# Performance work log

Measured on AMD Instinct MI355X. Metric: run time of the kernel, lower is better.

The kernel has to match this reference:

```python
import jax, jax.numpy as jnp
import numpy as np

BATCH = 8
MAX_SEQ = 2048
HEAD_NUM = 16  # num_attention_heads_per_partition


def setup_inputs() -> dict:
    key = jax.random.key(0)
    k1, k2 = jax.random.split(key)
    attention_mask = jax.random.uniform(k1, (BATCH, 1, MAX_SEQ, MAX_SEQ), dtype=jnp.float16)
    # ragged per-sequence lengths in [1, MAX_SEQ]; concrete (shape params, not traced)
    seq_lengths = np.asarray(jax.random.randint(k2, (BATCH,), 1, MAX_SEQ + 1), dtype=np.int32)
    return {"attention_mask": attention_mask, "seq_lengths": seq_lengths}


def reference(attention_mask, seq_lengths):
    # Pack the top-left s_i x s_i block of each batch's mask, replicated across
    # HEAD_NUM heads, into one flat fp16 buffer; then threshold > 0.5 -> bool.
    mask = attention_mask.astype(jnp.float16)
    lens = [int(s) for s in np.asarray(seq_lengths)]  # static shape params
    pieces = []
    for i, s in enumerate(lens):
        block = mask[i, 0, :s, :s]                        # [s, s]
        rep = jnp.broadcast_to(block, (HEAD_NUM, s, s))   # replicate per head
        pieces.append(rep.reshape(-1))                    # [HEAD_NUM*s*s]
    packed = jnp.concatenate(pieces)                      # [sum_i HEAD_NUM*s_i^2]
    return packed > jnp.float16(0.5)
```

## Files before the change

### kernel.cpp

```cpp
#include <hip/hip_runtime.h>

typedef int i4 __attribute__((ext_vector_type(4)));
typedef int i2 __attribute__((ext_vector_type(2)));

#define NTS4(P, V) __builtin_nontemporal_store((V), (i4*)(P))
#define NTS2(P, V) __builtin_nontemporal_store((V), (i2*)(P))
#define NTS1(P, V) __builtin_nontemporal_store((V), (P))

#define THREADS 256
#define WAVES_PB 4
#define ITERS 2
#define MAX_BLOCKS 4096

__global__ void setup_offsets_kernel(const int* __restrict__ seq,
                                     unsigned int* __restrict__ ws) {
    if (threadIdx.x == 0 && blockIdx.x == 0) {
        unsigned int o16 = 0, cs = 0;
        ws[0] = 0u; ws[9] = 0u;
        for (int b = 0; b < 8; ++b) {
            unsigned int s  = (unsigned int)seq[b];
            unsigned int s2 = s * s;
            o16 += 16u * s2;
            cs  += (s2 + 1023u) >> 10;
            ws[1 + b]  = o16;
            ws[10 + b] = cs;
            ws[18 + b] = s;
            ws[26 + b] = s2;
            ((float*)ws)[34 + b] = 1.0f / (float)s;
        }
    }
}

#define STORE_SHIFT(VV, SIG) do {                                              \
    NTS4(out + offh + 0   + (SIG), VV[0]);                                     \
    NTS4(out + offh + 256 + (SIG), VV[1]);                                     \
    NTS4(out + offh + 512 + (SIG), VV[2]);                                     \
    if (lane < 63u) NTS4(out + offh + 768 + (SIG), VV[3]);                     \
    if (lane == 0u) {                                                          \
        NTS1(out + habase, o[0].x);                                            \
        if ((SIG) >= 2) NTS1(out + habase + 1, o[0].y);                        \
        if ((SIG) == 3) NTS1(out + habase + 2, o[0].z);                        \
    }                                                                          \
    if (lane == 63u) {                                                         \
        if ((SIG) == 1) NTS1(out + habase + 1021, o[3].y);                     \
        if ((SIG) <= 2) NTS1(out + habase + 1022, o[3].z);                     \
        NTS1(out + habase + 1023, o[3].w);                                     \
    }                                                                          \
} while (0)

__global__ void __launch_bounds__(THREADS)
unpad_mask_kernel(const float* __restrict__ mask,
                  const unsigned int* __restrict__ ws,
                  int* __restrict__ out) {
    __shared__ unsigned int off16[9];
    __shared__ unsigned int csum[9];
    __shared__ unsigned int slen[8];
    __shared__ unsigned int ssq[8];
    __shared__ float        sinv[8];

    int tx = threadIdx.x;
    if (tx < 9) { off16[tx] = ws[tx]; csum[tx] = ws[9 + tx]; }
    if (tx < 8) {
        slen[tx] = ws[18 + tx];
        ssq[tx]  = ws[26 + tx];
        sinv[tx] = ((const float*)ws)[34 + tx];
    }
    __syncthreads();

    unsigned int nchunks     = csum[8];
    unsigned int total_waves = gridDim.x * WAVES_PB;
    unsigned int wave_id     = blockIdx.x * WAVES_PB + ((unsigned int)tx >> 6);
    unsigned int lane        = (unsigned int)tx & 63u;

#pragma unroll 1
    for (int it = 0; it < ITERS; ++it) {
        unsigned int chunk = wave_id + (unsigned int)it * total_waves;
        if (chunk >= nchunks) break;

        unsigned int b = 0;
#pragma unroll
        for (int j = 1; j < 8; ++j) b += (chunk >= csum[j]) ? 1u : 0u;

        unsigned int s    = slen[b];
        unsigned int s2   = ssq[b];
        float        inv  = sinv[b];
        unsigned int p0   = (chunk - csum[b]) << 10;
        unsigned int base = off16[b];
        const float* mb   = mask + ((size_t)b << 22);

        if (s2 - p0 >= 1024u) {
            unsigned int q0 = p0 + (lane << 2);
            i4 o[4];
#pragma unroll
            for (int sub = 0; sub < 4; ++sub) {
                unsigned int q   = q0 + ((unsigned int)sub << 8);
                unsigned int row = (unsigned int)((float)q * inv);
                int col = (int)q - (int)(row * s);
                if (col < 0)            { row -= 1u; col += (int)s; }
                else if (col >= (int)s) { row += 1u; col -= (int)s; }

                unsigned int r0 = row;  int c0 = col;
                float v0 = mb[(size_t)r0 * 2048u + (unsigned int)c0];
                c0++; if (c0 == (int)s) { c0 = 0; r0++; }
                float v1 = mb[(size_t)r0 * 2048u + (unsigned int)c0];
                c0++; if (c0 == (int)s) { c0 = 0; r0++; }
                float v2 = mb[(size_t)r0 * 2048u + (unsigned int)c0];
                c0++; if (c0 == (int)s) { c0 = 0; r0++; }
                float v3 = mb[(size_t)r0 * 2048u + (unsigned int)c0];

                o[sub] = (i4){(v0 > 0.5f) ? 1 : 0,
                              (v1 > 0.5f) ? 1 : 0,
                              (v2 > 0.5f) ? 1 : 0,
                              (v3 > 0.5f) ? 1 : 0};
            }

            if ((s & 1u) == 0u) {
                unsigned int off = base + q0;
#pragma unroll
                for (int h = 0; h < 16; ++h) {
                    NTS4(out + off,       o[0]);
                    NTS4(out + off + 256, o[1]);
                    NTS4(out + off + 512, o[2]);
                    NTS4(out + off + 768, o[3]);
                    off += s2;
                }
            } else {
                int src = ((int)lane + 1) & 63;
                int sel = (lane == 0u) ? 1 : 0;
                int e0x = sel ? o[1].x : o[0].x;
                int e0y = sel ? o[1].y : o[0].y;
                int e0z = sel ? o[1].z : o[0].z;
                int e1x = sel ? o[2].x : o[1].x;
                int e1y = sel ? o[2].y : o[1].y;
                int e1z = sel ? o[2].z : o[1].z;
                int e2x = sel ? o[3].x : o[2].x;
                int e2y = sel ? o[3].y : o[2].y;
                int e2z = sel ? o[3].z : o[2].z;
                int n0x = __shfl(e0x, src, 64), n0y = __shfl(e0y, src, 64), n0z = __shfl(e0z, src, 64);
                int n1x = __shfl(e1x, src, 64), n1y = __shfl(e1y, src, 64), n1z = __shfl(e1z, src, 64);
                int n2x = __shfl(e2x, src, 64), n2y = __shfl(e2y, src, 64), n2z = __shfl(e2z, src, 64);
                int n3x = __shfl(o[3].x, src, 64), n3y = __shfl(o[3].y, src, 64), n3z = __shfl(o[3].z, src, 64);

                i4 v1[4], v2[4], v3[4];
                v1[0] = (i4){o[0].y, o[0].z, o[0].w, n0x};
                v1[1] = (i4){o[1].y, o[1].z, o[1].w, n1x};
                v1[2] = (i4){o[2].y, o[2].z, o[2].w, n2x};
                v1[3] = (i4){o[3].y, o[3].z, o[3].w, n3x};
                v2[0] = (i4){o[0].z, o[0].w, n0x, n0y};
                v2[1] = (i4){o[1].z, o[1].w, n1x, n1y};
                v2[2] = (i4){o[2].z, o[2].w, n2x, n2y};
                v2[3] = (i4){o[3].z, o[3].w, n3x, n3y};
                v3[0] = (i4){o[0].w, n0x, n0y, n0z};
                v3[1] = (i4){o[1].w, n1x, n1y, n1z};
                v3[2] = (i4){o[2].w, n2x, n2y, n2z};
                v3[3] = (i4){o[3].w, n3x, n3y, n3z};

                unsigned int habase = base + p0;
#pragma unroll
                for (int h = 0; h < 16; ++h) {
                    unsigned int offh = habase + (lane << 2);
                    const int r0c = h & 3;
                    if (r0c == 0) {
                        NTS4(out + offh,       o[0]);
                        NTS4(out + offh + 256, o[1]);
                        NTS4(out + offh + 512, o[2]);
                        NTS4(out + offh + 768, o[3]);
                    } else if (r0c == 1) {
                        STORE_SHIFT(v3, 3);
                    } else if (r0c == 2) {
                        STORE_SHIFT(v2, 2);
                    } else {
                        STORE_SHIFT(v1, 1);
                    }
                    habase += s2;
                }
            }
        } else {
#pragma unroll 1
            for (int sub = 0; sub < 4; ++sub) {
                unsigned int sp0 = p0 + ((unsigned int)sub << 8);
                if (sp0 >= s2) break;

                if (s2 - sp0 >= 256u) {
                    unsigned int q   = sp0 + (lane << 2);
                    unsigned int row = (unsigned int)((float)q * inv);
                    int col = (int)q - (int)(row * s);
                    if (col < 0)            { row -= 1u; col += (int)s; }
                    else if (col >= (int)s) { row += 1u; col -= (int)s; }

                    unsigned int r0 = row;  int c0 = col;
                    float v0 = mb[(size_t)r0 * 2048u + (unsigned int)c0];
                    c0++; if (c0 == (int)s) { c0 = 0; r0++; }
                    float v1 = mb[(size_t)r0 * 2048u + (unsigned int)c0];
                    c0++; if (c0 == (int)s) { c0 = 0; r0++; }
                    float v2 = mb[(size_t)r0 * 2048u + (unsigned int)c0];
                    c0++; if (c0 == (int)s) { c0 = 0; r0++; }
                    float v3 = mb[(size_t)r0 * 2048u + (unsigned int)c0];

                    int o0 = (v0 > 0.5f) ? 1 : 0;
                    int o1 = (v1 > 0.5f) ? 1 : 0;
                    int o2 = (v2 > 0.5f) ? 1 : 0;
                    int o3 = (v3 > 0.5f) ? 1 : 0;
                    i4 o4  = (i4){o0, o1, o2, o3};
                    i2 o2a = (i2){o0, o1};
                    i2 o2b = (i2){o2, o3};

                    unsigned int off = base + q;
                    if ((s & 1u) == 0u) {
#pragma unroll
                        for (int h = 0; h < 16; ++h) {
                            NTS4(out + off, o4);
                            off += s2;
                        }
                    } else {
#pragma unroll
                        for (int h = 0; h < 16; ++h) {
                            if ((h & 3) == 0) {
                                NTS4(out + off, o4);
                            } else if ((h & 3) == 2) {
                                NTS2(out + off,     o2a);
                                NTS2(out + off + 2, o2b);
                            } else {
                                NTS1(out + off,     o0);
                                NTS1(out + off + 1, o1);
                                NTS1(out + off + 2, o2);
                                NTS1(out + off + 3, o3);
                            }
                            off += s2;
                        }
                    }
                } else {
#pragma unroll
                    for (int j = 0; j < 4; ++j) {
                        unsigned int p = sp0 + (lane << 2) + (unsigned int)j;
                        if (p >= s2) continue;
                        unsigned int row = (unsigned int)((float)p * inv);
                        int col = (int)p - (int)(row * s);
                        if (col < 0)            { row -= 1u; col += (int)s; }
                        else if (col >= (int)s) { row += 1u; col -= (int)s; }
                        float v = mb[(size_t)row * 2048u + (unsigned int)col];
                        int o = (v > 0.5f) ? 1 : 0;
                        unsigned int off = base + p;
#pragma unroll
                        for (int h = 0; h < 16; ++h) {
                            NTS1(out + off, o);
                            off += s2;
                        }
                    }
                }
            }
        }
    }
}

extern "C" void kernel_launch(void* const* d_in, const int* in_sizes, int n_in,
                              void* d_out, int out_size, void* d_ws, size_t ws_size,
                              hipStream_t stream) {
    const float*  mask = (const float*)d_in[0];
    const int*    seq  = (const int*)d_in[1];
    unsigned int* ws   = (unsigned int*)d_ws;
    int*          out  = (int*)d_out;

    setup_offsets_kernel<<<1, 64, 0, stream>>>(seq, ws);
    unpad_mask_kernel<<<MAX_BLOCKS, THREADS, 0, stream>>>(mask, ws, out);
}
```

Measured before the change: 680.6 us.

## Split mask unpad into pack pass and aligned per-head fanout copy kernel

Replaces the single fused kernel with two passes when workspace is large enough. The first pass thresholds and packs each sequence's mask block into a compact workspace buffer, and the second copies it out to all 16 head positions using aligned 16-byte output stores with scalar edge handling. This avoids the misaligned shuffle and split-store paths for odd sequence lengths, at the cost of an extra kernel launch and a packed intermediate that is written and then re-read. It also swaps the nontemporal stores for ordinary stores, and the old fused kernel stays as a fallback.

```diff
diff --git a/kernel.cpp b/kernel.cpp
--- a/kernel.cpp
+++ b/kernel.cpp
@@ -1,16 +1,16 @@
 #include <hip/hip_runtime.h>
 
-typedef int i4 __attribute__((ext_vector_type(4)));
-typedef int i2 __attribute__((ext_vector_type(2)));
-
-#define NTS4(P, V) __builtin_nontemporal_store((V), (i4*)(P))
-#define NTS2(P, V) __builtin_nontemporal_store((V), (i2*)(P))
-#define NTS1(P, V) __builtin_nontemporal_store((V), (P))
+typedef int i4  __attribute__((ext_vector_type(4)));
+typedef int i2  __attribute__((ext_vector_type(2)));
+typedef int i4u __attribute__((ext_vector_type(4), aligned(4)));
 
 #define THREADS 256
 #define WAVES_PB 4
-#define ITERS 2
-#define MAX_BLOCKS 4096
+#define K1_BLOCKS 4096
+#define K1_ITERS 2
+#define K2_BLOCKS 8192
+#define PK_OFF 256
+#define WS_NEED ((size_t)4 * (PK_OFF + 32768u * 1024u))
 
 __global__ void setup_offsets_kernel(const int* __restrict__ seq,
                                      unsigned int* __restrict__ ws) {
@@ -31,27 +31,157 @@
     }
 }
 
+
+__global__ void __launch_bounds__(THREADS)
+pack_kernel(const float* __restrict__ mask, const unsigned int* __restrict__ ws,
+            int* __restrict__ pk) {
+    __shared__ unsigned int csum[9];
+    __shared__ unsigned int slen[8];
+    __shared__ unsigned int ssq[8];
+    __shared__ float        sinv[8];
+    int tx = threadIdx.x;
+    if (tx < 9) csum[tx] = ws[9 + tx];
+    if (tx < 8) {
+        slen[tx] = ws[18 + tx];
+        ssq[tx]  = ws[26 + tx];
+        sinv[tx] = ((const float*)ws)[34 + tx];
+    }
+    __syncthreads();
+
+    unsigned int nchunks     = csum[8];
+    unsigned int total_waves = gridDim.x * WAVES_PB;
+    unsigned int wave_id     = blockIdx.x * WAVES_PB + ((unsigned int)tx >> 6);
+    unsigned int lane        = (unsigned int)tx & 63u;
+
+#pragma unroll 1
+    for (int it = 0; it < K1_ITERS; ++it) {
+        unsigned int chunk = wave_id + (unsigned int)it * total_waves;
+        if (chunk >= nchunks) break;
+
+        unsigned int b = 0;
+#pragma unroll
+        for (int j = 1; j < 8; ++j) b += (chunk >= csum[j]) ? 1u : 0u;
+
+        unsigned int s   = slen[b];
+        unsigned int s2  = ssq[b];
+        float        inv = sinv[b];
+        unsigned int p0  = (chunk - csum[b]) << 10;
+        unsigned int pb  = csum[b] << 10;
+        const float* mb  = mask + ((size_t)b << 22);
+
+#pragma unroll
+        for (int sub = 0; sub < 4; ++sub) {
+            unsigned int p = p0 + ((unsigned int)sub << 8) + (lane << 2);
+            if (p + 4u <= s2) {
+                unsigned int row = (unsigned int)((float)p * inv);
+                int col = (int)p - (int)(row * s);
+                if (col < 0)            { row -= 1u; col += (int)s; }
+                else if (col >= (int)s) { row += 1u; col -= (int)s; }
+                unsigned int r0 = row;  int c0 = col;
+                float v0 = mb[(size_t)r0 * 2048u + (unsigned int)c0];
+                c0++; if (c0 == (int)s) { c0 = 0; r0++; }
+                float v1 = mb[(size_t)r0 * 2048u + (unsigned int)c0];
+                c0++; if (c0 == (int)s) { c0 = 0; r0++; }
+                float v2 = mb[(size_t)r0 * 2048u + (unsigned int)c0];
+                c0++; if (c0 == (int)s) { c0 = 0; r0++; }
+                float v3 = mb[(size_t)r0 * 2048u + (unsigned int)c0];
+                i4 o = (i4){(v0 > 0.5f) ? 1 : 0, (v1 > 0.5f) ? 1 : 0,
+                            (v2 > 0.5f) ? 1 : 0, (v3 > 0.5f) ? 1 : 0};
+                *(i4*)(pk + pb + p) = o;
+            } else {
+#pragma unroll
+                for (int j = 0; j < 4; ++j) {
+                    unsigned int pp = p + (unsigned int)j;
+                    if (pp >= s2) continue;
+                    unsigned int row = (unsigned int)((float)pp * inv);
+                    int col = (int)pp - (int)(row * s);
+                    if (col < 0)            { row -= 1u; col += (int)s; }
+                    else if (col >= (int)s) { row += 1u; col -= (int)s; }
+                    float v = mb[(size_t)row * 2048u + (unsigned int)col];
+                    pk[pb + pp] = (v > 0.5f) ? 1 : 0;
+                }
+            }
+        }
+    }
+}
+
+__global__ void __launch_bounds__(THREADS)
+fanout_kernel(const unsigned int* __restrict__ ws, const int* __restrict__ pk,
+              int* __restrict__ out) {
+    __shared__ unsigned int off16[9];
+    __shared__ unsigned int csum[9];
+    __shared__ unsigned int ssq[8];
+    int tx = threadIdx.x;
+    if (tx < 9) { off16[tx] = ws[tx]; csum[tx] = ws[9 + tx]; }
+    if (tx < 8) ssq[tx] = ws[26 + tx];
+    __syncthreads();
+
+    unsigned int nitems      = csum[8] << 4;
+    unsigned int total_waves = gridDim.x * WAVES_PB;
+    unsigned int W           = blockIdx.x * WAVES_PB + ((unsigned int)tx >> 6);
+    unsigned int lane        = (unsigned int)tx & 63u;
+
+#pragma unroll 1
+    for (unsigned int item = W; item < nitems; item += total_waves) {
+        unsigned int cid = item >> 4;
+        unsigned int h   = item & 15u;
+
+        unsigned int b = 0;
+#pragma unroll
+        for (int j = 1; j < 8; ++j) b += (cid >= csum[j]) ? 1u : 0u;
+
+        unsigned int s2 = ssq[b];
+        unsigned int c  = cid - csum[b];
+        const int*  srcb = pk + (csum[b] << 10);
+
+        unsigned int hb   = off16[b] + h * s2;
+        unsigned int lo   = hb + (c << 10);
+        unsigned int clen = s2 - (c << 10);
+        if (clen > 1024u) clen = 1024u;
+        unsigned int hi = lo + clen;
+
+        unsigned int qs = (lo + 3u) >> 2;
+        unsigned int qe = hi >> 2;
+
+#pragma unroll
+        for (int k = 0; k < 4; ++k) {
+            unsigned int q = qs + lane + ((unsigned int)k << 6);
+            if (q < qe) {
+                i4 v = *(const i4u*)(srcb + ((q << 2) - hb));
+                *(i4*)(out + ((size_t)q << 2)) = v;
+            }
+        }
+        if (lane < 3u) {
+            unsigned int e = lo + lane;
+            if (e < hi && e < (qs << 2)) out[e] = srcb[e - hb];
+            unsigned int e2 = (qe << 2) + lane;
+            if (e2 >= lo && e2 < hi) out[e2] = srcb[e2 - hb];
+        }
+    }
+}
+
+
 #define STORE_SHIFT(VV, SIG) do {                                              \
-    NTS4(out + offh + 0   + (SIG), VV[0]);                                     \
-    NTS4(out + offh + 256 + (SIG), VV[1]);                                     \
-    NTS4(out + offh + 512 + (SIG), VV[2]);                                     \
-    if (lane < 63u) NTS4(out + offh + 768 + (SIG), VV[3]);                     \
+    *(i4*)(out + offh + 0   + (SIG)) = VV[0];                                  \
+    *(i4*)(out + offh + 256 + (SIG)) = VV[1];                                  \
+    *(i4*)(out + offh + 512 + (SIG)) = VV[2];                                  \
+    if (lane < 63u) *(i4*)(out + offh + 768 + (SIG)) = VV[3];                  \
     if (lane == 0u) {                                                          \
-        NTS1(out + habase, o[0].x);                                            \
-        if ((SIG) >= 2) NTS1(out + habase + 1, o[0].y);                        \
-        if ((SIG) == 3) NTS1(out + habase + 2, o[0].z);                        \
+        out[habase] = o[0].x;                                                  \
+        if ((SIG) >= 2) out[habase + 1] = o[0].y;                              \
+        if ((SIG) == 3) out[habase + 2] = o[0].z;                              \
     }                                                                          \
     if (lane == 63u) {                                                         \
-        if ((SIG) == 1) NTS1(out + habase + 1021, o[3].y);                     \
-        if ((SIG) <= 2) NTS1(out + habase + 1022, o[3].z);                     \
-        NTS1(out + habase + 1023, o[3].w);                                     \
+        if ((SIG) == 1) out[habase + 1021] = o[3].y;                           \
+        if ((SIG) <= 2) out[habase + 1022] = o[3].z;                           \
+        out[habase + 1023] = o[3].w;                                           \
     }                                                                          \
 } while (0)
 
 __global__ void __launch_bounds__(THREADS)
-unpad_mask_kernel(const float* __restrict__ mask,
-                  const unsigned int* __restrict__ ws,
-                  int* __restrict__ out) {
+unpad_mask_kernel_fb(const float* __restrict__ mask,
+                     const unsigned int* __restrict__ ws,
+                     int* __restrict__ out) {
     __shared__ unsigned int off16[9];
     __shared__ unsigned int csum[9];
     __shared__ unsigned int slen[8];
@@ -73,7 +203,7 @@
     unsigned int lane        = (unsigned int)tx & 63u;
 
 #pragma unroll 1
-    for (int it = 0; it < ITERS; ++it) {
+    for (int it = 0; it < K1_ITERS; ++it) {
         unsigned int chunk = wave_id + (unsigned int)it * total_waves;
         if (chunk >= nchunks) break;
 
@@ -98,7 +228,6 @@
                 int col = (int)q - (int)(row * s);
                 if (col < 0)            { row -= 1u; col += (int)s; }
                 else if (col >= (int)s) { row += 1u; col -= (int)s; }
-
                 unsigned int r0 = row;  int c0 = col;
                 float v0 = mb[(size_t)r0 * 2048u + (unsigned int)c0];
                 c0++; if (c0 == (int)s) { c0 = 0; r0++; }
@@ -107,21 +236,18 @@
                 float v2 = mb[(size_t)r0 * 2048u + (unsigned int)c0];
                 c0++; if (c0 == (int)s) { c0 = 0; r0++; }
                 float v3 = mb[(size_t)r0 * 2048u + (unsigned int)c0];
-
-                o[sub] = (i4){(v0 > 0.5f) ? 1 : 0,
-                              (v1 > 0.5f) ? 1 : 0,
-                              (v2 > 0.5f) ? 1 : 0,
-                              (v3 > 0.5f) ? 1 : 0};
+                o[sub] = (i4){(v0 > 0.5f) ? 1 : 0, (v1 > 0.5f) ? 1 : 0,
+                              (v2 > 0.5f) ? 1 : 0, (v3 > 0.5f) ? 1 : 0};
             }
 
             if ((s & 1u) == 0u) {
                 unsigned int off = base + q0;
 #pragma unroll
                 for (int h = 0; h < 16; ++h) {
-                    NTS4(out + off,       o[0]);
-                    NTS4(out + off + 256, o[1]);
-                    NTS4(out + off + 512, o[2]);
-                    NTS4(out + off + 768, o[3]);
+                    *(i4*)(out + off)       = o[0];
+                    *(i4*)(out + off + 256) = o[1];
+                    *(i4*)(out + off + 512) = o[2];
+                    *(i4*)(out + off + 768) = o[3];
                     off += s2;
                 }
             } else {
@@ -161,10 +287,10 @@
                     unsigned int offh = habase + (lane << 2);
                     const int r0c = h & 3;
                     if (r0c == 0) {
-                        NTS4(out + offh,       o[0]);
-                        NTS4(out + offh + 256, o[1]);
-                        NTS4(out + offh + 512, o[2]);
-                        NTS4(out + offh + 768, o[3]);
+                        *(i4*)(out + offh)       = o[0];
+                        *(i4*)(out + offh + 256) = o[1];
+                        *(i4*)(out + offh + 512) = o[2];
+                        *(i4*)(out + offh + 768) = o[3];
                     } else if (r0c == 1) {
                         STORE_SHIFT(v3, 3);
                     } else if (r0c == 2) {
@@ -180,72 +306,21 @@
             for (int sub = 0; sub < 4; ++sub) {
                 unsigned int sp0 = p0 + ((unsigned int)sub << 8);
                 if (sp0 >= s2) break;
-
-                if (s2 - sp0 >= 256u) {
-                    unsigned int q   = sp0 + (lane << 2);
-                    unsigned int row = (unsigned int)((float)q * inv);
-                    int col = (int)q - (int)(row * s);
+#pragma unroll
+                for (int j = 0; j < 4; ++j) {
+                    unsigned int p = sp0 + (lane << 2) + (unsigned int)j;
+                    if (p >= s2) continue;
+                    unsigned int row = (unsigned int)((float)p * inv);
+                    int col = (int)p - (int)(row * s);
                     if (col < 0)            { row -= 1u; col += (int)s; }
                     else if (col >= (int)s) { row += 1u; col -= (int)s; }
-
-                    unsigned int r0 = row;  int c0 = col;
-                    float v0 = mb[(size_t)r0 * 2048u + (unsigned int)c0];
-                    c0++; if (c0 == (int)s) { c0 = 0; r0++; }
-                    float v1 = mb[(size_t)r0 * 2048u + (unsigned int)c0];
-                    c0++; if (c0 == (int)s) { c0 = 0; r0++; }
-                    float v2 = mb[(size_t)r0 * 2048u + (unsigned int)c0];
-                    c0++; if (c0 == (int)s) { c0 = 0; r0++; }
-                    float v3 = mb[(size_t)r0 * 2048u + (unsigned int)c0];
-
-                    int o0 = (v0 > 0.5f) ? 1 : 0;
-                    int o1 = (v1 > 0.5f) ? 1 : 0;
-                    int o2 = (v2 > 0.5f) ? 1 : 0;
-                    int o3 = (v3 > 0.5f) ? 1 : 0;
-                    i4 o4  = (i4){o0, o1, o2, o3};
-                    i2 o2a = (i2){o0, o1};
-                    i2 o2b = (i2){o2, o3};
-
-                    unsigned int off = base + q;
-                    if ((s & 1u) == 0u) {
-#pragma unroll
-                        for (int h = 0; h < 16; ++h) {
-                            NTS4(out + off, o4);
-                            off += s2;
-                        }
-                    } else {
-#pragma unroll
-                        for (int h = 0; h < 16; ++h) {
-                            if ((h & 3) == 0) {
-                                NTS4(out + off, o4);
-                            } else if ((h & 3) == 2) {
-                                NTS2(out + off,     o2a);
-                                NTS2(out + off + 2, o2b);
-                            } else {
-                                NTS1(out + off,     o0);
-                                NTS1(out + off + 1, o1);
-                                NTS1(out + off + 2, o2);
-                                NTS1(out + off + 3, o3);
-                            }
-                            off += s2;
-                        }
-                    }
-                } else {
-#pragma unroll
-                    for (int j = 0; j < 4; ++j) {
-                        unsigned int p = sp0 + (lane << 2) + (unsigned int)j;
-                        if (p >= s2) continue;
-                        unsigned int row = (unsigned int)((float)p * inv);
-                        int col = (int)p - (int)(row * s);
-                        if (col < 0)            { row -= 1u; col += (int)s; }
-                        else if (col >= (int)s) { row += 1u; col -= (int)s; }
-                        float v = mb[(size_t)row * 2048u + (unsigned int)col];
-                        int o = (v > 0.5f) ? 1 : 0;
-                        unsigned int off = base + p;
-#pragma unroll
-                        for (int h = 0; h < 16; ++h) {
-                            NTS1(out + off, o);
-                            off += s2;
-                        }
+                    float v = mb[(size_t)row * 2048u + (unsigned int)col];
+                    int o = (v > 0.5f) ? 1 : 0;
+                    unsigned int off = base + p;
+#pragma unroll
+                    for (int h = 0; h < 16; ++h) {
+                        out[off] = o;
+                        off += s2;
                     }
                 }
             }
@@ -262,5 +337,11 @@
     int*          out  = (int*)d_out;
 
     setup_offsets_kernel<<<1, 64, 0, stream>>>(seq, ws);
-    unpad_mask_kernel<<<MAX_BLOCKS, THREADS, 0, stream>>>(mask, ws, out);
-}
+    if (ws_size >= WS_NEED) {
+        int* pk = (int*)ws + PK_OFF;
+        pack_kernel<<<K1_BLOCKS, THREADS, 0, stream>>>(mask, ws, pk);
+        fanout_kernel<<<K2_BLOCKS, THREADS, 0, stream>>>(ws, pk, out);
+    } else {
+        unpad_mask_kernel_fb<<<K1_BLOCKS, THREADS, 0, stream>>>(mask, ws, out);
+    }
+}
```

Result: slower. 724.6 us (+6.5%).

## Fold offset setup into main kernel and use regular stores

Applied to the files above, without the earlier changes.

Removes the separate single-thread setup kernel: each block's thread 0 now computes the per-batch offsets, chunk prefix sums, lengths and inverse lengths from the sequence lengths directly into shared memory. This drops one kernel launch and the global workspace round trip. All nontemporal stores are also replaced with ordinary stores, so output writes go through the normal cache path. The trade-off is a short serial prologue per block and possible cache pollution from the large output stream.

```diff
diff --git a/kernel.cpp b/kernel.cpp
--- a/kernel.cpp
+++ b/kernel.cpp
@@ -2,55 +2,32 @@
 
 typedef int i4 __attribute__((ext_vector_type(4)));
 typedef int i2 __attribute__((ext_vector_type(2)));
-
-#define NTS4(P, V) __builtin_nontemporal_store((V), (i4*)(P))
-#define NTS2(P, V) __builtin_nontemporal_store((V), (i2*)(P))
-#define NTS1(P, V) __builtin_nontemporal_store((V), (P))
 
 #define THREADS 256
 #define WAVES_PB 4
 #define ITERS 2
 #define MAX_BLOCKS 4096
 
-__global__ void setup_offsets_kernel(const int* __restrict__ seq,
-                                     unsigned int* __restrict__ ws) {
-    if (threadIdx.x == 0 && blockIdx.x == 0) {
-        unsigned int o16 = 0, cs = 0;
-        ws[0] = 0u; ws[9] = 0u;
-        for (int b = 0; b < 8; ++b) {
-            unsigned int s  = (unsigned int)seq[b];
-            unsigned int s2 = s * s;
-            o16 += 16u * s2;
-            cs  += (s2 + 1023u) >> 10;
-            ws[1 + b]  = o16;
-            ws[10 + b] = cs;
-            ws[18 + b] = s;
-            ws[26 + b] = s2;
-            ((float*)ws)[34 + b] = 1.0f / (float)s;
-        }
-    }
-}
-
 #define STORE_SHIFT(VV, SIG) do {                                              \
-    NTS4(out + offh + 0   + (SIG), VV[0]);                                     \
-    NTS4(out + offh + 256 + (SIG), VV[1]);                                     \
-    NTS4(out + offh + 512 + (SIG), VV[2]);                                     \
-    if (lane < 63u) NTS4(out + offh + 768 + (SIG), VV[3]);                     \
+    *(i4*)(out + offh + 0   + (SIG)) = VV[0];                                  \
+    *(i4*)(out + offh + 256 + (SIG)) = VV[1];                                  \
+    *(i4*)(out + offh + 512 + (SIG)) = VV[2];                                  \
+    if (lane < 63u) *(i4*)(out + offh + 768 + (SIG)) = VV[3];                  \
     if (lane == 0u) {                                                          \
-        NTS1(out + habase, o[0].x);                                            \
-        if ((SIG) >= 2) NTS1(out + habase + 1, o[0].y);                        \
-        if ((SIG) == 3) NTS1(out + habase + 2, o[0].z);                        \
+        out[habase] = o[0].x;                                                  \
+        if ((SIG) >= 2) out[habase + 1] = o[0].y;                              \
+        if ((SIG) == 3) out[habase + 2] = o[0].z;                              \
     }                                                                          \
     if (lane == 63u) {                                                         \
-        if ((SIG) == 1) NTS1(out + habase + 1021, o[3].y);                     \
-        if ((SIG) <= 2) NTS1(out + habase + 1022, o[3].z);                     \
-        NTS1(out + habase + 1023, o[3].w);                                     \
+        if ((SIG) == 1) out[habase + 1021] = o[3].y;                           \
+        if ((SIG) <= 2) out[habase + 1022] = o[3].z;                           \
+        out[habase + 1023] = o[3].w;                                           \
     }                                                                          \
 } while (0)
 
 __global__ void __launch_bounds__(THREADS)
 unpad_mask_kernel(const float* __restrict__ mask,
-                  const unsigned int* __restrict__ ws,
+                  const int* __restrict__ seq,
                   int* __restrict__ out) {
     __shared__ unsigned int off16[9];
     __shared__ unsigned int csum[9];
@@ -59,11 +36,21 @@
     __shared__ float        sinv[8];
 
     int tx = threadIdx.x;
-    if (tx < 9) { off16[tx] = ws[tx]; csum[tx] = ws[9 + tx]; }
-    if (tx < 8) {
-        slen[tx] = ws[18 + tx];
-        ssq[tx]  = ws[26 + tx];
-        sinv[tx] = ((const float*)ws)[34 + tx];
+    if (tx == 0) {
+        unsigned int o16 = 0, cs = 0;
+        off16[0] = 0u; csum[0] = 0u;
+#pragma unroll
+        for (int b = 0; b < 8; ++b) {
+            unsigned int s  = (unsigned int)seq[b];
+            unsigned int s2 = s * s;
+            o16 += s2 << 4;
+            cs  += (s2 + 1023u) >> 10;
+            off16[b + 1] = o16;
+            csum[b + 1]  = cs;
+            slen[b] = s;
+            ssq[b]  = s2;
+            sinv[b] = 1.0f / (float)s;
+        }
     }
     __syncthreads();
 
@@ -108,20 +95,18 @@
                 c0++; if (c0 == (int)s) { c0 = 0; r0++; }
                 float v3 = mb[(size_t)r0 * 2048u + (unsigned int)c0];
 
-                o[sub] = (i4){(v0 > 0.5f) ? 1 : 0,
-                              (v1 > 0.5f) ? 1 : 0,
-                              (v2 > 0.5f) ? 1 : 0,
-                              (v3 > 0.5f) ? 1 : 0};
+                o[sub] = (i4){(v0 > 0.5f) ? 1 : 0, (v1 > 0.5f) ? 1 : 0,
+                              (v2 > 0.5f) ? 1 : 0, (v3 > 0.5f) ? 1 : 0};
             }
 
             if ((s & 1u) == 0u) {
                 unsigned int off = base + q0;
 #pragma unroll
                 for (int h = 0; h < 16; ++h) {
-                    NTS4(out + off,       o[0]);
-                    NTS4(out + off + 256, o[1]);
-                    NTS4(out + off + 512, o[2]);
-                    NTS4(out + off + 768, o[3]);
+                    *(i4*)(out + off)       = o[0];
+                    *(i4*)(out + off + 256) = o[1];
+                    *(i4*)(out + off + 512) = o[2];
+                    *(i4*)(out + off + 768) = o[3];
                     off += s2;
                 }
             } else {
@@ -161,10 +146,10 @@
                     unsigned int offh = habase + (lane << 2);
                     const int r0c = h & 3;
                     if (r0c == 0) {
-                        NTS4(out + offh,       o[0]);
-                        NTS4(out + offh + 256, o[1]);
-                        NTS4(out + offh + 512, o[2]);
-                        NTS4(out + offh + 768, o[3]);
+                        *(i4*)(out + offh)       = o[0];
+                        *(i4*)(out + offh + 256) = o[1];
+                        *(i4*)(out + offh + 512) = o[2];
+                        *(i4*)(out + offh + 768) = o[3];
                     } else if (r0c == 1) {
                         STORE_SHIFT(v3, 3);
                     } else if (r0c == 2) {
@@ -209,22 +194,22 @@
                     if ((s & 1u) == 0u) {
 #pragma unroll
                         for (int h = 0; h < 16; ++h) {
-                            NTS4(out + off, o4);
+                            *(i4*)(out + off) = o4;
                             off += s2;
                         }
                     } else {
 #pragma unroll
                         for (int h = 0; h < 16; ++h) {
                             if ((h & 3) == 0) {
-                                NTS4(out + off, o4);
+                                *(i4*)(out + off) = o4;
                             } else if ((h & 3) == 2) {
-                                NTS2(out + off,     o2a);
-                                NTS2(out + off + 2, o2b);
+                                *(i2*)(out + off)     = o2a;
+                                *(i2*)(out + off + 2) = o2b;
                             } else {
-                                NTS1(out + off,     o0);
-                                NTS1(out + off + 1, o1);
-                                NTS1(out + off + 2, o2);
-                                NTS1(out + off + 3, o3);
+                                out[off]     = o0;
+                                out[off + 1] = o1;
+                                out[off + 2] = o2;
+                                out[off + 3] = o3;
                             }
                             off += s2;
                         }
@@ -243,7 +228,7 @@
                         unsigned int off = base + p;
 #pragma unroll
                         for (int h = 0; h < 16; ++h) {
-                            NTS1(out + off, o);
+                            out[off] = o;
                             off += s2;
                         }
                     }
@@ -256,11 +241,10 @@
 extern "C" void kernel_launch(void* const* d_in, const int* in_sizes, int n_in,
                               void* d_out, int out_size, void* d_ws, size_t ws_size,
                               hipStream_t stream) {
-    const float*  mask = (const float*)d_in[0];
-    const int*    seq  = (const int*)d_in[1];
-    unsigned int* ws   = (unsigned int*)d_ws;
-    int*          out  = (int*)d_out;
-
-    setup_offsets_kernel<<<1, 64, 0, stream>>>(seq, ws);
-    unpad_mask_kernel<<<MAX_BLOCKS, THREADS, 0, stream>>>(mask, ws, out);
+    const float* mask = (const float*)d_in[0];
+    const int*   seq  = (const int*)d_in[1];
+    int*         out  = (int*)d_out;
+    (void)d_ws; (void)ws_size;
+
+    unpad_mask_kernel<<<MAX_BLOCKS, THREADS, 0, stream>>>(mask, seq, out);
 }
```

New measurement: 660.5 us. -2.9%, faster.
